# Optimization experiments

Hardware: AMD Instinct MI355X
Metric: run time of the kernel (lower is better)

## Reference

```python
import jax, jax.numpy as jnp
import numpy as np

H = 16  # n_heads
D = 64  # d_keys


def setup_inputs() -> dict:
    key = jax.random.key(0)
    ks = jax.random.split(key, 11)
    b, n, dm = 2, 2048, 1024
    s = 1.0 / np.sqrt(dm)
    return {
        "q": jax.random.normal(ks[0], (b, n, dm), jnp.float32),
        "k": jax.random.normal(ks[1], (b, n, dm), jnp.float32),
        "v": jax.random.normal(ks[2], (b, n, dm), jnp.float32),
        "Wq": jax.random.normal(ks[3], (dm, H * D), jnp.float32) * s,
        "bq": jax.random.normal(ks[4], (H * D,), jnp.float32) * 0.01,
        "Wk": jax.random.normal(ks[5], (dm, H * D), jnp.float32) * s,
        "bk": jax.random.normal(ks[6], (H * D,), jnp.float32) * 0.01,
        "Wv": jax.random.normal(ks[7], (dm, H * D), jnp.float32) * s,
        "bv": jax.random.normal(ks[8], (H * D,), jnp.float32) * 0.01,
        "Wo": jax.random.normal(ks[9], (H * D, dm), jnp.float32) * s,
        "bo": jax.random.normal(ks[10], (dm,), jnp.float32) * 0.01,
    }


def reference(q, k, v, Wq, bq, Wk, bk, Wv, bv, Wo, bo):
    b, n_q, _ = q.shape
    n_k = k.shape[1]
    # projections -> [b, n, h, d]
    qh = (q @ Wq + bq).reshape(b, n_q, H, D)
    kh = (k @ Wk + bk).reshape(b, n_k, H, D)
    vh = (v @ Wv + bv).reshape(b, n_k, H, D)
    # scores [b, h, n, m]
    scores = jnp.einsum('bnhd,bmhd->bhnm', qh, kh)
    causal = jnp.triu(jnp.ones((n_q, n_k), dtype=bool), k=1)  # True above diag
    scores = jnp.where(causal, -jnp.inf, scores)
    att = jax.nn.softmax(scores / np.sqrt(D).astype(np.float32), axis=-1)
    att_out = jnp.einsum('bhnm,bmhd->bnhd', att, vh).reshape(b, n_q, H * D)
    return att_out @ Wo + bo
```

## Files before the change

### kernel.cpp

```cpp
#include <hip/hip_runtime.h>

typedef float f32x4 __attribute__((ext_vector_type(4)));
typedef __bf16 bf16x8 __attribute__((ext_vector_type(8)));
typedef __bf16 bf16x4 __attribute__((ext_vector_type(4)));
typedef __bf16 bf16_t;

#define NH 16
#define DH 64
#define SEQ 2048
#define DM 1024

extern "C" hipError_t hipMemPtrGetInfo(void* ptr, size_t* size);

__device__ __forceinline__ bf16x8 ld8(const bf16_t* p) { return *(const bf16x8*)p; }
__device__ __forceinline__ void st8(bf16_t* p, bf16x8 v) { *(bf16x8*)p = v; }

__device__ __forceinline__ void gl_lds16(const bf16_t* g, bf16_t* l)
{
    __builtin_amdgcn_global_load_lds(
        (const __attribute__((address_space(1))) unsigned int*)g,
        (__attribute__((address_space(3))) unsigned int*)l, 16, 0, 0);
}

__global__ __launch_bounds__(256) void fill_sentinel(float* out, unsigned n, float val)
{
    unsigned stride = gridDim.x * blockDim.x;
    for (unsigned i = blockIdx.x * blockDim.x + threadIdx.x; i < n; i += stride)
        out[i] = val;
}

__global__ __launch_bounds__(256) void prep(
    const float* __restrict__ q, const float* __restrict__ k,
    const float* __restrict__ v,
    const float* __restrict__ w0, const float* __restrict__ w1,
    const float* __restrict__ w2, const float* __restrict__ w3,
    bf16_t* __restrict__ xb, bf16_t* __restrict__ wt)
{
    int z = blockIdx.z;
    if (z < 3) {
        const float* src = (z == 0) ? q : (z == 1) ? k : v;
        bf16_t* dst = xb + (size_t)z * (4096u * 1024u);
        size_t i8 = ((size_t)blockIdx.x * 256 + threadIdx.x) * 8;
        f32x4 u = *(const f32x4*)(src + i8);
        f32x4 w = *(const f32x4*)(src + i8 + 4);
        bf16x8 h = { (bf16_t)u.x, (bf16_t)u.y, (bf16_t)u.z, (bf16_t)u.w,
                     (bf16_t)w.x, (bf16_t)w.y, (bf16_t)w.z, (bf16_t)w.w };
        st8(dst + i8, h);
    } else {
        int x = blockIdx.x;
        if (x >= 1024) return;
        int w = x >> 8, rem = x & 255;
        int bx = rem & 15, by = rem >> 4;
        const float* in = (w == 0) ? w0 : (w == 1) ? w1 : (w == 2) ? w2 : w3;
        bf16_t* out = wt + (size_t)w * DM * DM;
        __shared__ __align__(16) bf16_t tile[64][72];
        int t = threadIdx.x;
        int k0 = by * 64, n0 = bx * 64;
        int r0 = t >> 4, c0 = (t & 15) * 4;
        for (int p = 0; p < 4; p++) {
            int r = r0 + p * 16;
            const float* src = in + (size_t)(k0 + r) * DM + n0 + c0;
            for (int i = 0; i < 4; i++) tile[r][c0 + i] = (bf16_t)src[i];
        }
        __syncthreads();
        for (int p = 0; p < 4; p++) {
            int rn = r0 + p * 16;
            bf16_t* dst = out + (size_t)(n0 + rn) * DM + k0 + c0;
            for (int i = 0; i < 4; i++) dst[i] = tile[c0 + i][rn];
        }
    }
}

__device__ __forceinline__ void gemm_epilogue(
    f32x4 (&acc)[4][4], const float* bias, bf16_t* out, float* outf,
    int mode, int out_is_f32, int m0, int n0, int wr0, int wc0, int g, int l16)
{
    float scale = (mode == 0) ? 0.125f : 1.0f;
    for (int mi = 0; mi < 4; mi++) {
        int mbase = m0 + wr0 + mi * 16 + g * 4;
        for (int ni = 0; ni < 4; ni++) {
            int col = n0 + wc0 + ni * 16 + l16;
            float bv = bias[col];
            if (mode == 2) {
                int bb = mbase >> 11, nn0 = mbase & 2047;
                int h = col >> 6, d = col & 63;
                bf16x4 pv;
                for (int r = 0; r < 4; r++) pv[r] = (bf16_t)(acc[mi][ni][r] + bv);
                *(bf16x4*)(out + ((size_t)(bb * NH + h) * DH + d) * SEQ + nn0) = pv;
            } else {
                for (int r = 0; r < 4; r++) {
                    int mr = mbase + r;
                    float sv = (acc[mi][ni][r] + bv) * scale;
                    if (mode == 3) {
                        if (out_is_f32) outf[(size_t)mr * 1024 + col] = sv;
                        else            out[(size_t)mr * 1024 + col] = (bf16_t)sv;
                    } else {
                        int bb = mr >> 11, nn = mr & 2047;
                        int h = col >> 6, d = col & 63;
                        out[((size_t)(bb * NH + h) * SEQ + nn) * DH + d] = (bf16_t)sv;
                    }
                }
            }
        }
    }
}

__global__ __launch_bounds__(256) void gemm_fast(
    const bf16_t* __restrict__ xb_base, const bf16_t* __restrict__ wt_base,
    const float* __restrict__ b0, const float* __restrict__ b1,
    const float* __restrict__ b2, bf16_t* __restrict__ out_base,
    float* __restrict__ outf, int mode_base, int out_is_f32)
{
    int z = blockIdx.z;
    const bf16_t* X    = xb_base + (size_t)z * (4096u * 1024u);
    const bf16_t* WT   = wt_base + (size_t)z * DM * DM;
    const float* bias  = (z == 0) ? b0 : (z == 1) ? b1 : b2;
    bf16_t* out = out_base + (size_t)z * (4096u * 1024u);
    int mode = mode_base + z;

    int m0 = blockIdx.x * 128;
    int n0 = blockIdx.y * 128;

    __shared__ __align__(16) bf16_t Alds[128 * 64];
    __shared__ __align__(16) bf16_t Blds[128 * 64];

    int t = threadIdx.x;
    int lane = t & 63, wave = t >> 6;
    int g = lane >> 4, l16 = lane & 15;
    int wr0 = (wave >> 1) * 64, wc0 = (wave & 1) * 64;
    int crow = lane >> 3;
    int ccol = (lane & 7) * 8;

    f32x4 acc[4][4] = {};

    for (int k0 = 0; k0 < DM; k0 += 64) {
        __syncthreads();
        for (int c = wave; c < 16; c += 4) {
            int row = c * 8 + crow;
            gl_lds16(X  + (size_t)(m0 + row) * DM + k0 + ccol,
                     Alds + c * 512 + lane * 8);
            gl_lds16(WT + (size_t)(n0 + row) * DM + k0 + ccol,
                     Blds + c * 512 + lane * 8);
        }
        __syncthreads();
        for (int kk = 0; kk < 2; kk++) {
            bf16x8 af[4], bfr[4];
            for (int i = 0; i < 4; i++)
                af[i] = ld8(Alds + (wr0 + i * 16 + l16) * 64 + kk * 32 + g * 8);
            for (int i = 0; i < 4; i++)
                bfr[i] = ld8(Blds + (wc0 + i * 16 + l16) * 64 + kk * 32 + g * 8);
            for (int mi = 0; mi < 4; mi++)
                for (int ni = 0; ni < 4; ni++)
                    acc[mi][ni] = __builtin_amdgcn_mfma_f32_16x16x32_bf16(
                        af[mi], bfr[ni], acc[mi][ni], 0, 0, 0);
        }
    }
    gemm_epilogue(acc, bias, out, outf, mode, out_is_f32, m0, n0, wr0, wc0, g, l16);
}

__global__ __launch_bounds__(256) void gemm_mha(
    const float* __restrict__ x0, const float* __restrict__ x1,
    const float* __restrict__ x2, const bf16_t* __restrict__ xb,
    const bf16_t* __restrict__ wt_base,
    const float* __restrict__ b0, const float* __restrict__ b1,
    const float* __restrict__ b2, bf16_t* __restrict__ out_base,
    float* __restrict__ outf, int mode_base, int out_is_f32)
{
    int z = blockIdx.z;
    const float* Xf    = (z == 0) ? x0 : (z == 1) ? x1 : x2;
    const bf16_t* WT   = wt_base + (size_t)z * DM * DM;
    const float* bias  = (z == 0) ? b0 : (z == 1) ? b1 : b2;
    bf16_t* out = out_base + (size_t)z * (4096u * 1024u);
    int mode = mode_base + z;

    int m0 = blockIdx.x * 128;
    int n0 = blockIdx.y * 128;

    __shared__ __align__(16) bf16_t Alds[128 * 64];
    __shared__ __align__(16) bf16_t Blds[128 * 64];

    int t = threadIdx.x;
    int lane = t & 63, wave = t >> 6;
    int g = lane >> 4, l16 = lane & 15;
    int wr0 = (wave >> 1) * 64, wc0 = (wave & 1) * 64;

    f32x4 acc[4][4] = {};
    int srow = t >> 3, sk = (t & 7) * 8;

    for (int k0 = 0; k0 < DM; k0 += 64) {
        __syncthreads();
        if (mode < 3) {
            for (int p = 0; p < 4; p++) {
                int r = srow + p * 32;
                const float* s4 = Xf + (size_t)(m0 + r) * DM + k0 + sk;
                f32x4 u = *(const f32x4*)s4;
                f32x4 w = *(const f32x4*)(s4 + 4);
                bf16x8 h = { (bf16_t)u.x, (bf16_t)u.y, (bf16_t)u.z, (bf16_t)u.w,
                             (bf16_t)w.x, (bf16_t)w.y, (bf16_t)w.z, (bf16_t)w.w };
                st8(Alds + r * 64 + sk, h);
            }
        } else {
            for (int p = 0; p < 4; p++) {
                int r = srow + p * 32;
                st8(Alds + r * 64 + sk, ld8(xb + (size_t)(m0 + r) * DM + k0 + sk));
            }
        }
        for (int p = 0; p < 4; p++) {
            int r = srow + p * 32;
            st8(Blds + r * 64 + sk, ld8(WT + (size_t)(n0 + r) * DM + k0 + sk));
        }
        __syncthreads();
        for (int kk = 0; kk < 2; kk++) {
            bf16x8 af[4], bfr[4];
            for (int i = 0; i < 4; i++)
                af[i] = ld8(Alds + (wr0 + i * 16 + l16) * 64 + kk * 32 + g * 8);
            for (int i = 0; i < 4; i++)
                bfr[i] = ld8(Blds + (wc0 + i * 16 + l16) * 64 + kk * 32 + g * 8);
            for (int mi = 0; mi < 4; mi++)
                for (int ni = 0; ni < 4; ni++)
                    acc[mi][ni] = __builtin_amdgcn_mfma_f32_16x16x32_bf16(
                        af[mi], bfr[ni], acc[mi][ni], 0, 0, 0);
        }
    }
    gemm_epilogue(acc, bias, out, outf, mode, out_is_f32, m0, n0, wr0, wc0, g, l16);
}

__global__ __launch_bounds__(512) void attn(
    const bf16_t* __restrict__ Qh, const bf16_t* __restrict__ Kh,
    const bf16_t* __restrict__ VT, bf16_t* __restrict__ att)
{
    int bhx = blockIdx.x;
    int yy  = blockIdx.y;
    int p   = (yy < 8) ? yy : 23 - yy;
    int TB  = 2 * p + 2;

    const bf16_t* Qb = Qh + (size_t)bhx * SEQ * DH;
    const bf16_t* Kb = Kh + (size_t)bhx * SEQ * DH;
    const bf16_t* Vb = VT + (size_t)bhx * DH * SEQ;

    __shared__ __align__(16) bf16_t Klds[2][64 * 72];
    __shared__ __align__(16) bf16_t Vlds[2][64 * 72];
    __shared__ __align__(16) bf16_t Plds[8][16 * 72];

    int t = threadIdx.x, lane = t & 63, wave = t >> 6;
    int g = lane >> 4, l16 = lane & 15;
    int srow = t >> 3, sk = (t & 7) * 8;
    int qt = 2 * p + (wave >> 2);
    int Tw = qt + 1;
    int rowl = (wave & 3) * 16 + l16;

    bf16x8 qf[2];
    for (int kk = 0; kk < 2; kk++)
        qf[kk] = ld8(Qb + (size_t)(qt * 64 + rowl) * DH + kk * 32 + g * 8);

    f32x4 accO[4] = {};
    float l = 0.f;
    bf16_t* Pw = Plds[wave];

    st8(&Klds[0][srow * 72 + sk], ld8(Kb + (size_t)srow * DH + sk));
    st8(&Vlds[0][srow * 72 + sk], ld8(Vb + (size_t)srow * SEQ + sk));

    for (int j = 0; j < TB; j++) {
        __syncthreads();
        if (j + 1 < TB) {
            int b = (j + 1) & 1;
            st8(&Klds[b][srow * 72 + sk],
                ld8(Kb + (size_t)((j + 1) * 64 + srow) * DH + sk));
            st8(&Vlds[b][srow * 72 + sk],
                ld8(Vb + (size_t)srow * SEQ + (j + 1) * 64 + sk));
        }
        if (j >= Tw) continue;
        int buf = j & 1;
        bool diag = (j == Tw - 1);

        f32x4 s[4];
        for (int c = 0; c < 4; c++) {
            f32x4 a = {};
            for (int kk = 0; kk < 2; kk++) {
                bf16x8 kf = ld8(&Klds[buf][(c * 16 + l16) * 72 + kk * 32 + g * 8]);
                a = __builtin_amdgcn_mfma_f32_16x16x32_bf16(kf, qf[kk], a, 0, 0, 0);
            }
            s[c] = a;
        }
        for (int c = 0; c < 4; c++) {
            bf16x4 pv;
            for (int r = 0; r < 4; r++) {
                float v = s[c][r];
                if (diag && (c * 16 + g * 4 + r) > rowl) v = -1e30f;
                float pe = __expf(v);
                l += pe;
                pv[r] = (bf16_t)pe;
            }
            *(bf16x4*)(Pw + l16 * 72 + c * 16 + g * 4) = pv;
        }
        asm volatile("s_waitcnt lgkmcnt(0)" ::: "memory");

        bf16x8 pf0 = ld8(Pw + l16 * 72 + g * 8);
        bf16x8 pf1 = ld8(Pw + l16 * 72 + 32 + g * 8);
        for (int c2 = 0; c2 < 4; c2++) {
            bf16x8 vf0 = ld8(&Vlds[buf][(c2 * 16 + l16) * 72 + g * 8]);
            accO[c2] = __builtin_amdgcn_mfma_f32_16x16x32_bf16(vf0, pf0, accO[c2], 0, 0, 0);
            bf16x8 vf1 = ld8(&Vlds[buf][(c2 * 16 + l16) * 72 + 32 + g * 8]);
            accO[c2] = __builtin_amdgcn_mfma_f32_16x16x32_bf16(vf1, pf1, accO[c2], 0, 0, 0);
        }

        if (diag) {
            float lt = l;
            lt += __shfl_xor(lt, 16);
            lt += __shfl_xor(lt, 32);
            float inv = 1.f / lt;
            int qabs = qt * 64 + rowl;
            int bb = bhx >> 4, h = bhx & 15;
            for (int c2 = 0; c2 < 4; c2++) {
                bf16x4 ov;
                for (int r = 0; r < 4; r++) ov[r] = (bf16_t)(accO[c2][r] * inv);
                *(bf16x4*)(att + (((size_t)bb * SEQ + qabs) * NH + h) * DH
                           + c2 * 16 + g * 4) = ov;
            }
        }
    }
}

extern "C" void kernel_launch(void* const* d_in, const int* in_sizes, int n_in,
                              void* d_out, int out_size, void* d_ws, size_t ws_size,
                              hipStream_t stream) {
    const float* q  = (const float*)d_in[0];
    const float* k  = (const float*)d_in[1];
    const float* v  = (const float*)d_in[2];
    const float* Wq = (const float*)d_in[3];
    const float* bq = (const float*)d_in[4];
    const float* Wk = (const float*)d_in[5];
    const float* bk = (const float*)d_in[6];
    const float* Wv = (const float*)d_in[7];
    const float* bv = (const float*)d_in[8];
    const float* Wo = (const float*)d_in[9];
    const float* bo = (const float*)d_in[10];

    const size_t MAT = 1024u * 1024u;
    const size_t BIG = 4096u * 1024u;
    const size_t NEED_BASE = 64 + (4 * BIG + 4 * MAT) * 2;
    const size_t NEED_FAST = NEED_BASE + 3 * BIG * 2;

    if (ws_size < NEED_BASE) {
        fill_sentinel<<<1024, 256, 0, stream>>>((float*)d_out,
                                                (unsigned)out_size, 100.0f);
        return;
    }

    int out_is_f32 = 1;
    size_t osz = 0;
    if (hipMemPtrGetInfo(d_out, &osz) == hipSuccess && osz != 0 &&
        osz < (size_t)out_size * 4)
        out_is_f32 = 0;

    bf16_t* base = (bf16_t*)d_ws + 32;
    bf16_t* Qh  = base;
    bf16_t* Kh  = Qh + BIG;
    bf16_t* VT  = Kh + BIG;
    bf16_t* att = VT + BIG;
    bf16_t* WT  = att + BIG;
    bf16_t* Xb  = WT + 4 * MAT;

    if (ws_size >= NEED_FAST) {
        prep<<<dim3(2048, 1, 4), 256, 0, stream>>>(q, k, v, Wq, Wk, Wv, Wo, Xb, WT);
        gemm_fast<<<dim3(32, 8, 3), 256, 0, stream>>>(Xb, WT, bq, bk, bv,
                                                      Qh, nullptr, 0, 0);
        attn<<<dim3(32, 16), 512, 0, stream>>>(Qh, Kh, VT, att);
        gemm_fast<<<dim3(32, 8, 1), 256, 0, stream>>>(att, WT + 3 * MAT,
                                                      bo, bo, bo,
                                                      (bf16_t*)d_out, (float*)d_out,
                                                      3, out_is_f32);
    } else {
        prep<<<dim3(2048, 1, 4), 256, 0, stream>>>(q, k, v, Wq, Wk, Wv, Wo,
                                                   (bf16_t*)d_ws, WT);
        gemm_mha<<<dim3(32, 8, 3), 256, 0, stream>>>(q, k, v, nullptr, WT,
                                                     bq, bk, bv, Qh, nullptr, 0, 0);
        attn<<<dim3(32, 16), 512, 0, stream>>>(Qh, Kh, VT, att);
        gemm_mha<<<dim3(32, 8, 1), 256, 0, stream>>>(nullptr, nullptr, nullptr, att,
                                                     WT + 3 * MAT, bo, bo, bo,
                                                     (bf16_t*)d_out, (float*)d_out,
                                                     3, out_is_f32);
    }
}
```

Before: 244.9 us.

## Fuse fp32-to-bf16 input conversion into projection GEMM with register prefetch

```diff
diff --git a/kernel.cpp b/kernel.cpp
--- a/kernel.cpp
+++ b/kernel.cpp
@@ -15,13 +15,6 @@
 __device__ __forceinline__ bf16x8 ld8(const bf16_t* p) { return *(const bf16x8*)p; }
 __device__ __forceinline__ void st8(bf16_t* p, bf16x8 v) { *(bf16x8*)p = v; }
 
-__device__ __forceinline__ void gl_lds16(const bf16_t* g, bf16_t* l)
-{
-    __builtin_amdgcn_global_load_lds(
-        (const __attribute__((address_space(1))) unsigned int*)g,
-        (__attribute__((address_space(3))) unsigned int*)l, 16, 0, 0);
-}
-
 __global__ __launch_bounds__(256) void fill_sentinel(float* out, unsigned n, float val)
 {
     unsigned stride = gridDim.x * blockDim.x;
@@ -29,45 +22,28 @@
         out[i] = val;
 }
 
-__global__ __launch_bounds__(256) void prep(
-    const float* __restrict__ q, const float* __restrict__ k,
-    const float* __restrict__ v,
+__global__ __launch_bounds__(256) void transpose_w(
     const float* __restrict__ w0, const float* __restrict__ w1,
     const float* __restrict__ w2, const float* __restrict__ w3,
-    bf16_t* __restrict__ xb, bf16_t* __restrict__ wt)
+    bf16_t* __restrict__ out_base)
 {
     int z = blockIdx.z;
-    if (z < 3) {
-        const float* src = (z == 0) ? q : (z == 1) ? k : v;
-        bf16_t* dst = xb + (size_t)z * (4096u * 1024u);
-        size_t i8 = ((size_t)blockIdx.x * 256 + threadIdx.x) * 8;
-        f32x4 u = *(const f32x4*)(src + i8);
-        f32x4 w = *(const f32x4*)(src + i8 + 4);
-        bf16x8 h = { (bf16_t)u.x, (bf16_t)u.y, (bf16_t)u.z, (bf16_t)u.w,
-                     (bf16_t)w.x, (bf16_t)w.y, (bf16_t)w.z, (bf16_t)w.w };
-        st8(dst + i8, h);
-    } else {
-        int x = blockIdx.x;
-        if (x >= 1024) return;
-        int w = x >> 8, rem = x & 255;
-        int bx = rem & 15, by = rem >> 4;
-        const float* in = (w == 0) ? w0 : (w == 1) ? w1 : (w == 2) ? w2 : w3;
-        bf16_t* out = wt + (size_t)w * DM * DM;
-        __shared__ __align__(16) bf16_t tile[64][72];
-        int t = threadIdx.x;
-        int k0 = by * 64, n0 = bx * 64;
-        int r0 = t >> 4, c0 = (t & 15) * 4;
-        for (int p = 0; p < 4; p++) {
-            int r = r0 + p * 16;
-            const float* src = in + (size_t)(k0 + r) * DM + n0 + c0;
-            for (int i = 0; i < 4; i++) tile[r][c0 + i] = (bf16_t)src[i];
-        }
-        __syncthreads();
-        for (int p = 0; p < 4; p++) {
-            int rn = r0 + p * 16;
-            bf16_t* dst = out + (size_t)(n0 + rn) * DM + k0 + c0;
-            for (int i = 0; i < 4; i++) dst[i] = tile[c0 + i][rn];
-        }
+    const float* in = (z == 0) ? w0 : (z == 1) ? w1 : (z == 2) ? w2 : w3;
+    bf16_t* out = out_base + (size_t)z * DM * DM;
+    __shared__ __align__(16) bf16_t tile[64][72];
+    int t = threadIdx.x;
+    int k0 = blockIdx.y * 64, n0 = blockIdx.x * 64;
+    int r0 = t >> 4, c0 = (t & 15) * 4;
+    for (int p = 0; p < 4; p++) {
+        int r = r0 + p * 16;
+        const float* src = in + (size_t)(k0 + r) * DM + n0 + c0;
+        for (int i = 0; i < 4; i++) tile[r][c0 + i] = (bf16_t)src[i];
+    }
+    __syncthreads();
+    for (int p = 0; p < 4; p++) {
+        int rn = r0 + p * 16;
+        bf16_t* dst = out + (size_t)(n0 + rn) * DM + k0 + c0;
+        for (int i = 0; i < 4; i++) dst[i] = tile[c0 + i][rn];
     }
 }
 
@@ -105,14 +81,16 @@
     }
 }
 
-__global__ __launch_bounds__(256) void gemm_fast(
-    const bf16_t* __restrict__ xb_base, const bf16_t* __restrict__ wt_base,
+__global__ __launch_bounds__(256) void gemm_pf(
+    const float* __restrict__ x0, const float* __restrict__ x1,
+    const float* __restrict__ x2, const bf16_t* __restrict__ xb,
+    const bf16_t* __restrict__ wt_base,
     const float* __restrict__ b0, const float* __restrict__ b1,
     const float* __restrict__ b2, bf16_t* __restrict__ out_base,
     float* __restrict__ outf, int mode_base, int out_is_f32)
 {
     int z = blockIdx.z;
-    const bf16_t* X    = xb_base + (size_t)z * (4096u * 1024u);
+    const float* Xf    = (z == 0) ? x0 : (z == 1) ? x1 : x2;
     const bf16_t* WT   = wt_base + (size_t)z * DM * DM;
     const float* bias  = (z == 0) ? b0 : (z == 1) ? b1 : b2;
     bf16_t* out = out_base + (size_t)z * (4096u * 1024u);
@@ -128,21 +106,45 @@
     int lane = t & 63, wave = t >> 6;
     int g = lane >> 4, l16 = lane & 15;
     int wr0 = (wave >> 1) * 64, wc0 = (wave & 1) * 64;
-    int crow = lane >> 3;
-    int ccol = (lane & 7) * 8;
+
+    int srow = t >> 1;
+    int scol = (t & 1) * 32;
+
+    f32x4 aF[8];
+    bf16x8 aH[4];
+    bf16x8 bH[4];
+
+    const float*  Ap32 = (mode < 3) ? Xf + (size_t)(m0 + srow) * DM + scol : nullptr;
+    const bf16_t* Ap16 = (mode == 3) ? xb + (size_t)(m0 + srow) * DM + scol : nullptr;
+    const bf16_t* Bp   = WT + (size_t)(n0 + srow) * DM + scol;
+
+    if (mode < 3) { for (int i = 0; i < 8; i++) aF[i] = *(const f32x4*)(Ap32 + i * 4); }
+    else          { for (int i = 0; i < 4; i++) aH[i] = ld8(Ap16 + i * 8); }
+    for (int i = 0; i < 4; i++) bH[i] = ld8(Bp + i * 8);
 
     f32x4 acc[4][4] = {};
 
     for (int k0 = 0; k0 < DM; k0 += 64) {
+        if (mode < 3) {
+            for (int i = 0; i < 4; i++) {
+                f32x4 u = aF[2 * i], w = aF[2 * i + 1];
+                bf16x8 h = { (bf16_t)u.x, (bf16_t)u.y, (bf16_t)u.z, (bf16_t)u.w,
+                             (bf16_t)w.x, (bf16_t)w.y, (bf16_t)w.z, (bf16_t)w.w };
+                st8(Alds + srow * 64 + scol + i * 8, h);
+            }
+        } else {
+            for (int i = 0; i < 4; i++) st8(Alds + srow * 64 + scol + i * 8, aH[i]);
+        }
+        for (int i = 0; i < 4; i++) st8(Blds + srow * 64 + scol + i * 8, bH[i]);
         __syncthreads();
-        for (int c = wave; c < 16; c += 4) {
-            int row = c * 8 + crow;
-            gl_lds16(X  + (size_t)(m0 + row) * DM + k0 + ccol,
-                     Alds + c * 512 + lane * 8);
-            gl_lds16(WT + (size_t)(n0 + row) * DM + k0 + ccol,
-                     Blds + c * 512 + lane * 8);
-        }
-        __syncthreads();
+
+        if (k0 + 64 < DM) {
+            int kn = k0 + 64;
+            if (mode < 3) { for (int i = 0; i < 8; i++) aF[i] = *(const f32x4*)(Ap32 + kn + i * 4); }
+            else          { for (int i = 0; i < 4; i++) aH[i] = ld8(Ap16 + kn + i * 8); }
+            for (int i = 0; i < 4; i++) bH[i] = ld8(Bp + kn + i * 8);
+        }
+
         for (int kk = 0; kk < 2; kk++) {
             bf16x8 af[4], bfr[4];
             for (int i = 0; i < 4; i++)
@@ -154,73 +156,7 @@
                     acc[mi][ni] = __builtin_amdgcn_mfma_f32_16x16x32_bf16(
                         af[mi], bfr[ni], acc[mi][ni], 0, 0, 0);
         }
-    }
-    gemm_epilogue(acc, bias, out, outf, mode, out_is_f32, m0, n0, wr0, wc0, g, l16);
-}
-
-__global__ __launch_bounds__(256) void gemm_mha(
-    const float* __restrict__ x0, const float* __restrict__ x1,
-    const float* __restrict__ x2, const bf16_t* __restrict__ xb,
-    const bf16_t* __restrict__ wt_base,
-    const float* __restrict__ b0, const float* __restrict__ b1,
-    const float* __restrict__ b2, bf16_t* __restrict__ out_base,
-    float* __restrict__ outf, int mode_base, int out_is_f32)
-{
-    int z = blockIdx.z;
-    const float* Xf    = (z == 0) ? x0 : (z == 1) ? x1 : x2;
-    const bf16_t* WT   = wt_base + (size_t)z * DM * DM;
-    const float* bias  = (z == 0) ? b0 : (z == 1) ? b1 : b2;
-    bf16_t* out = out_base + (size_t)z * (4096u * 1024u);
-    int mode = mode_base + z;
-
-    int m0 = blockIdx.x * 128;
-    int n0 = blockIdx.y * 128;
-
-    __shared__ __align__(16) bf16_t Alds[128 * 64];
-    __shared__ __align__(16) bf16_t Blds[128 * 64];
-
-    int t = threadIdx.x;
-    int lane = t & 63, wave = t >> 6;
-    int g = lane >> 4, l16 = lane & 15;
-    int wr0 = (wave >> 1) * 64, wc0 = (wave & 1) * 64;
-
-    f32x4 acc[4][4] = {};
-    int srow = t >> 3, sk = (t & 7) * 8;
-
-    for (int k0 = 0; k0 < DM; k0 += 64) {
         __syncthreads();
-        if (mode < 3) {
-            for (int p = 0; p < 4; p++) {
-                int r = srow + p * 32;
-                const float* s4 = Xf + (size_t)(m0 + r) * DM + k0 + sk;
-                f32x4 u = *(const f32x4*)s4;
-                f32x4 w = *(const f32x4*)(s4 + 4);
-                bf16x8 h = { (bf16_t)u.x, (bf16_t)u.y, (bf16_t)u.z, (bf16_t)u.w,
-                             (bf16_t)w.x, (bf16_t)w.y, (bf16_t)w.z, (bf16_t)w.w };
-                st8(Alds + r * 64 + sk, h);
-            }
-        } else {
-            for (int p = 0; p < 4; p++) {
-                int r = srow + p * 32;
-                st8(Alds + r * 64 + sk, ld8(xb + (size_t)(m0 + r) * DM + k0 + sk));
-            }
-        }
-        for (int p = 0; p < 4; p++) {
-            int r = srow + p * 32;
-            st8(Blds + r * 64 + sk, ld8(WT + (size_t)(n0 + r) * DM + k0 + sk));
-        }
-        __syncthreads();
-        for (int kk = 0; kk < 2; kk++) {
-            bf16x8 af[4], bfr[4];
-            for (int i = 0; i < 4; i++)
-                af[i] = ld8(Alds + (wr0 + i * 16 + l16) * 64 + kk * 32 + g * 8);
-            for (int i = 0; i < 4; i++)
-                bfr[i] = ld8(Blds + (wc0 + i * 16 + l16) * 64 + kk * 32 + g * 8);
-            for (int mi = 0; mi < 4; mi++)
-                for (int ni = 0; ni < 4; ni++)
-                    acc[mi][ni] = __builtin_amdgcn_mfma_f32_16x16x32_bf16(
-                        af[mi], bfr[ni], acc[mi][ni], 0, 0, 0);
-        }
     }
     gemm_epilogue(acc, bias, out, outf, mode, out_is_f32, m0, n0, wr0, wc0, g, l16);
 }
@@ -338,10 +274,9 @@
 
     const size_t MAT = 1024u * 1024u;
     const size_t BIG = 4096u * 1024u;
-    const size_t NEED_BASE = 64 + (4 * BIG + 4 * MAT) * 2;
-    const size_t NEED_FAST = NEED_BASE + 3 * BIG * 2;
-
-    if (ws_size < NEED_BASE) {
+    const size_t NEED = 64 + (4 * BIG + 4 * MAT) * 2;
+
+    if (ws_size < NEED) {
         fill_sentinel<<<1024, 256, 0, stream>>>((float*)d_out,
                                                 (unsigned)out_size, 100.0f);
         return;
@@ -359,26 +294,13 @@
     bf16_t* VT  = Kh + BIG;
     bf16_t* att = VT + BIG;
     bf16_t* WT  = att + BIG;
-    bf16_t* Xb  = WT + 4 * MAT;
-
-    if (ws_size >= NEED_FAST) {
-        prep<<<dim3(2048, 1, 4), 256, 0, stream>>>(q, k, v, Wq, Wk, Wv, Wo, Xb, WT);
-        gemm_fast<<<dim3(32, 8, 3), 256, 0, stream>>>(Xb, WT, bq, bk, bv,
-                                                      Qh, nullptr, 0, 0);
-        attn<<<dim3(32, 16), 512, 0, stream>>>(Qh, Kh, VT, att);
-        gemm_fast<<<dim3(32, 8, 1), 256, 0, stream>>>(att, WT + 3 * MAT,
-                                                      bo, bo, bo,
-                                                      (bf16_t*)d_out, (float*)d_out,
-                                                      3, out_is_f32);
-    } else {
-        prep<<<dim3(2048, 1, 4), 256, 0, stream>>>(q, k, v, Wq, Wk, Wv, Wo,
-                                                   (bf16_t*)d_ws, WT);
-        gemm_mha<<<dim3(32, 8, 3), 256, 0, stream>>>(q, k, v, nullptr, WT,
-                                                     bq, bk, bv, Qh, nullptr, 0, 0);
-        attn<<<dim3(32, 16), 512, 0, stream>>>(Qh, Kh, VT, att);
-        gemm_mha<<<dim3(32, 8, 1), 256, 0, stream>>>(nullptr, nullptr, nullptr, att,
-                                                     WT + 3 * MAT, bo, bo, bo,
-                                                     (bf16_t*)d_out, (float*)d_out,
-                                                     3, out_is_f32);
-    }
-}
+
+    transpose_w<<<dim3(16, 16, 4), 256, 0, stream>>>(Wq, Wk, Wv, Wo, WT);
+    gemm_pf<<<dim3(32, 8, 3), 256, 0, stream>>>(q, k, v, nullptr, WT,
+                                                bq, bk, bv, Qh, nullptr, 0, 0);
+    attn<<<dim3(32, 16), 512, 0, stream>>>(Qh, Kh, VT, att);
+    gemm_pf<<<dim3(32, 8, 1), 256, 0, stream>>>(nullptr, nullptr, nullptr, att,
+                                                WT + 3 * MAT, bo, bo, bo,
+                                                (bf16_t*)d_out, (float*)d_out,
+                                                3, out_is_f32);
+}
```

Measured after the change: 276.8 us. +13.0%, slower.
